# Kernel optimization log

Measured on AMD Instinct MI355X. Metric: run time of the kernel, lower is better.

The kernel has to match this reference:

```python
import jax, jax.numpy as jnp
import numpy as np

N = 262144          # total atoms
B = 2048            # graphs (batch.max()+1)
HID = 256           # hidden
CND = 128           # cond_proj_dim
K = 16              # n_clusters
PH = 8              # pool_heads
DH = HID // PH      # head_dim


def setup_inputs() -> dict:
    key = jax.random.key(0)
    ks = jax.random.split(key, 20)
    s = 0.02
    inp = {
        "h_atom": jax.random.normal(ks[0], (N, HID), jnp.float32),
        "c_atom": jax.random.normal(ks[1], (N, CND), jnp.float32),
        "batch": jnp.sort(jax.random.randint(ks[2], (N,), 0, B)).astype(jnp.int64),
        # gate: Linear(HID+CND, HID) -> GELU -> Linear(HID, 1) -> Sigmoid
        "W1": jax.random.normal(ks[3], (HID + CND, HID), jnp.float32) * s,
        "b1": jnp.zeros((HID,), jnp.float32),
        "W2": jax.random.normal(ks[4], (HID, 1), jnp.float32) * s,
        "b2": jnp.zeros((1,), jnp.float32),
        # assign: Linear(HID, HID) -> GELU -> Linear(HID, K)
        "A1": jax.random.normal(ks[5], (HID, HID), jnp.float32) * s,
        "ab1": jnp.zeros((HID,), jnp.float32),
        "A2": jax.random.normal(ks[6], (HID, K), jnp.float32) * s,
        "ab2": jnp.zeros((K,), jnp.float32),
        # cluster_proj: Linear(HID, HID)
        "Wc": jax.random.normal(ks[7], (HID, HID), jnp.float32) * s,
        "bc": jnp.zeros((HID,), jnp.float32),
        # readout
        "q": jax.random.normal(ks[8], (PH, DH), jnp.float32),   # readout_q param
        "Wk": jax.random.normal(ks[9], (HID, HID), jnp.float32) * s,
        "Wv": jax.random.normal(ks[10], (HID, HID), jnp.float32) * s,
        # LayerNorm
        "gamma": jnp.ones((HID,), jnp.float32),
        "beta": jnp.zeros((HID,), jnp.float32),
    }
    return inp


def reference(h_atom, c_atom, batch, W1, b1, W2, b2, A1, ab1, A2, ab2,
              Wc, bc, q, Wk, Wv, gamma, beta):
    gelu = lambda x: jax.nn.gelu(x, approximate=False)  # torch default GELU (erf)
    # Stage 1: condition-aware gating
    g = gelu(jnp.concatenate([h_atom, c_atom], axis=-1) @ W1 + b1)
    alpha = jax.nn.sigmoid(g @ W2 + b2)                 # [N, 1]
    h_gated = alpha * h_atom                            # [N, HID]
    # Stage 2: soft cluster assignment
    S = jax.nn.softmax(gelu(h_gated @ A1 + ab1) @ A2 + ab2, axis=-1)  # [N, K]
    # Ragged per-graph segment matmul: cluster[b,k,:] = sum_{n in graph b} S[n,k] * h_gated[n,:]
    cluster = jnp.stack(
        [jax.ops.segment_sum(h_gated * S[:, k:k + 1], batch, num_segments=B)
         for k in range(K)], axis=1)                    # [B, K, HID]
    cluster = cluster @ Wc + bc                         # cluster_proj
    # Stage 3: multi-head attention readout over K clusters
    Kp = (cluster @ Wk).reshape(B, K, PH, DH)
    Vp = (cluster @ Wv).reshape(B, K, PH, DH)
    scale = DH ** -0.5
    logits = jnp.einsum('pd,bkpd->bpk', q, Kp) * scale  # [B, PH, K]
    w = jax.nn.softmax(logits, axis=-1)                 # dropout p=0 -> identity
    out = jnp.einsum('bpk,bkpd->bpd', w, Vp).reshape(B, HID)
    # LayerNorm (eps = 1e-5, torch default)
    mu = out.mean(axis=-1, keepdims=True)
    var = ((out - mu) ** 2).mean(axis=-1, keepdims=True)
    return (out - mu) * jax.lax.rsqrt(var + 1e-5) * gamma + beta
```

## Files before the change

### kernel.cpp

```cpp
#include <hip/hip_runtime.h>
#include <hip/hip_bf16.h>
#include <math.h>

#define NATOMS 262144
#define BGRAPH 2048

typedef __bf16 bf16_t;
typedef __bf16 bf16x8 __attribute__((ext_vector_type(8)));
typedef __bf16 bf16x4 __attribute__((ext_vector_type(4)));
typedef float f32x4 __attribute__((ext_vector_type(4)));

__device__ __forceinline__ float bf2f(bf16_t x){ return (float)x; }
__device__ __forceinline__ float gelu_f(float x){ return 0.5f*x*(1.0f+erff(x*0.70710678118654752f)); }

__global__ void bounds_kernel(const int* __restrict__ batch,
                              const unsigned* __restrict__ gamma,
                              int* __restrict__ starts, int* __restrict__ flags) {
    if (blockIdx.x == 0 && threadIdx.x == 0)
        flags[0] = (gamma[0] == 0x3F803F80u) ? 1 : 0;
    int b = blockIdx.x * 256 + threadIdx.x;
    if (b > BGRAPH) return;
    int is64 = (batch[NATOMS - 1] == 0) ? 1 : 0;
    int lo = 0, hi = NATOMS;
    while (lo < hi) {
        int mid = (lo + hi) >> 1;
        int v = is64 ? batch[2 * mid] : batch[mid];
        if (v < b) lo = mid + 1; else hi = mid;
    }
    starts[b] = lo;
}

__global__ void params_kernel(const void* b1, const void* W2, const void* ab1,
                              const void* bc, const void* q, const void* gamma,
                              const void* beta, const void* ab2, const void* b2,
                              float* __restrict__ P, const int* __restrict__ flags) {
    int t = threadIdx.x;
    int bf = flags[0];
#define CV(p,i) (bf ? bf2f(((const bf16_t*)(p))[i]) : ((const float*)(p))[i])
    P[t]        = CV(b1, t);
    P[256 + t]  = CV(W2, t);
    P[512 + t]  = CV(ab1, t);
    P[768 + t]  = CV(bc, t);
    P[1024 + t] = CV(q, t);
    P[1280 + t] = CV(gamma, t);
    P[1536 + t] = CV(beta, t);
    if (t < 16) P[1792 + t] = CV(ab2, t);
    if (t == 16) P[1808] = CV(b2, 0);
#undef CV
}

__global__ void chunk_transpose(const void* __restrict__ src, bf16_t* __restrict__ dst,
                                int Kd, int Nn, const int* __restrict__ flags) {
    int i = blockIdx.x * 256 + threadIdx.x;
    if (i >= Kd * Nn) return;
    int k = i / Nn, n = i - k * Nn;
    bf16_t v = flags[0] ? ((const bf16_t*)src)[i] : (bf16_t)(((const float*)src)[i]);
    dst[((size_t)(k >> 5) * Nn + n) * 32 + (k & 31)] = v;
}

__global__ void a2_transpose(const void* __restrict__ src, bf16_t* __restrict__ dst,
                             const int* __restrict__ flags) {
    int i = blockIdx.x * 256 + threadIdx.x;
    if (i >= 256 * 16) return;
    int k = i >> 4, n = i & 15;
    bf16_t v = flags[0] ? ((const bf16_t*)src)[i] : (bf16_t)(((const float*)src)[i]);
    dst[n * 256 + k] = v;
}

__global__ __launch_bounds__(256, 2) void atom_kernel(
    const void* __restrict__ h, const void* __restrict__ cnd,
    const bf16_t* __restrict__ W1c, const bf16_t* __restrict__ A1c,
    const bf16_t* __restrict__ A2t, const float* __restrict__ P,
    const int* __restrict__ flags,
    bf16_t* __restrict__ hg_out, float* __restrict__ S_out)
{
    __shared__ bf16_t ldsX[64 * 392];
    __shared__ bf16_t ldsW[256 * 40];
    __shared__ float  ldsV[256];
    __shared__ float  ldsB1[256];
    __shared__ float  ldsAB1[256];
    __shared__ float  ldsAlpha[64];

    const int tid  = threadIdx.x;
    const int wave = tid >> 6;
    const int lane = tid & 63;
    const int quad = lane >> 4;
    const int l15  = lane & 15;
    const int a0   = blockIdx.x * 64;
    const int dbf  = flags[0];

    ldsV[tid]   = P[256 + tid];
    ldsB1[tid]  = P[tid];
    ldsAB1[tid] = P[512 + tid];
    if (tid < 64) ldsAlpha[tid] = 0.f;
    const float b2v = P[1808];

    if (dbf) {
        const uint4* hs = (const uint4*)((const bf16_t*)h + (size_t)a0 * 256);
        for (int i = 0; i < 8; ++i) {
            int lin = i * 256 + tid; int row = lin >> 5; int off = lin & 31;
            *(uint4*)(&ldsX[row * 392 + off * 8]) = hs[row * 32 + off];
        }
        const uint4* cs = (const uint4*)((const bf16_t*)cnd + (size_t)a0 * 128);
        for (int i = 0; i < 4; ++i) {
            int lin = i * 256 + tid; int row = lin >> 4; int off = lin & 15;
            *(uint4*)(&ldsX[row * 392 + 256 + off * 8]) = cs[row * 16 + off];
        }
    } else {
        const float4* hs = (const float4*)((const float*)h + (size_t)a0 * 256);
        for (int i = 0; i < 16; ++i) {
            int lin = i * 256 + tid; int row = lin >> 6; int off = lin & 63;
            float4 v = hs[row * 64 + off];
            bf16x4 w = { (bf16_t)v.x, (bf16_t)v.y, (bf16_t)v.z, (bf16_t)v.w };
            *(bf16x4*)(&ldsX[row * 392 + off * 4]) = w;
        }
        const float4* cs = (const float4*)((const float*)cnd + (size_t)a0 * 128);
        for (int i = 0; i < 8; ++i) {
            int lin = i * 256 + tid; int row = lin >> 5; int off = lin & 31;
            float4 v = cs[row * 32 + off];
            bf16x4 w = { (bf16_t)v.x, (bf16_t)v.y, (bf16_t)v.z, (bf16_t)v.w };
            *(bf16x4*)(&ldsX[row * 392 + 256 + off * 4]) = w;
        }
    }
    __syncthreads();

    f32x4 acc[4][4];
    for (int a = 0; a < 4; ++a) for (int b = 0; b < 4; ++b) acc[a][b] = (f32x4){0.f,0.f,0.f,0.f};

    for (int ks = 0; ks < 12; ++ks) {
        const uint4* src = (const uint4*)(W1c + (size_t)ks * 8192);
        for (int i = 0; i < 4; ++i) {
            int lin = i * 256 + tid; int n = lin >> 2, p = lin & 3;
            *(uint4*)(&ldsW[n * 40 + p * 8]) = src[n * 4 + p];
        }
        __syncthreads();
        bf16x8 af[4], bv[4];
        int kb = ks * 32 + quad * 8;
        for (int mt = 0; mt < 4; ++mt) af[mt] = *(const bf16x8*)(&ldsX[(mt * 16 + l15) * 392 + kb]);
        for (int j = 0; j < 4; ++j)   bv[j]  = *(const bf16x8*)(&ldsW[(wave * 64 + j * 16 + l15) * 40 + quad * 8]);
        for (int mt = 0; mt < 4; ++mt)
            for (int j = 0; j < 4; ++j)
                acc[mt][j] = __builtin_amdgcn_mfma_f32_16x16x32_bf16(af[mt], bv[j], acc[mt][j], 0, 0, 0);
        __syncthreads();
    }

    for (int mt = 0; mt < 4; ++mt) {
        float p[4] = {0.f, 0.f, 0.f, 0.f};
        for (int j = 0; j < 4; ++j) {
            int col = wave * 64 + j * 16 + l15;
            float w = ldsV[col];
            float bb = ldsB1[col];
            for (int r = 0; r < 4; ++r) {
                float g = gelu_f(acc[mt][j][r] + bb);
                p[r] += g * w;
            }
        }
        for (int off = 1; off < 16; off <<= 1)
            for (int r = 0; r < 4; ++r) p[r] += __shfl_xor(p[r], off, 64);
        if (l15 == 0)
            for (int r = 0; r < 4; ++r)
                atomicAdd(&ldsAlpha[mt * 16 + quad * 4 + r], p[r]);
    }
    __syncthreads();

    {
        int r = tid >> 2, p4 = tid & 3;
        float al = 1.f / (1.f + expf(-(ldsAlpha[r] + b2v)));
        bf16_t* xrow = &ldsX[r * 392 + p4 * 64];
        bf16_t* grow = hg_out + (size_t)(a0 + r) * 256 + p4 * 64;
        for (int i = 0; i < 8; ++i) {
            bf16x8 v = *(bf16x8*)(xrow + i * 8);
            for (int e = 0; e < 8; ++e) v[e] = (bf16_t)(bf2f(v[e]) * al);
            *(bf16x8*)(xrow + i * 8) = v;
            *(bf16x8*)(grow + i * 8) = v;
        }
    }
    __syncthreads();

    for (int a = 0; a < 4; ++a) for (int b = 0; b < 4; ++b) acc[a][b] = (f32x4){0.f,0.f,0.f,0.f};
    for (int ks = 0; ks < 8; ++ks) {
        const uint4* src = (const uint4*)(A1c + (size_t)ks * 8192);
        for (int i = 0; i < 4; ++i) {
            int lin = i * 256 + tid; int n = lin >> 2, p = lin & 3;
            *(uint4*)(&ldsW[n * 40 + p * 8]) = src[n * 4 + p];
        }
        __syncthreads();
        bf16x8 af[4], bv[4];
        int kb = ks * 32 + quad * 8;
        for (int mt = 0; mt < 4; ++mt) af[mt] = *(const bf16x8*)(&ldsX[(mt * 16 + l15) * 392 + kb]);
        for (int j = 0; j < 4; ++j)   bv[j]  = *(const bf16x8*)(&ldsW[(wave * 64 + j * 16 + l15) * 40 + quad * 8]);
        for (int mt = 0; mt < 4; ++mt)
            for (int j = 0; j < 4; ++j)
                acc[mt][j] = __builtin_amdgcn_mfma_f32_16x16x32_bf16(af[mt], bv[j], acc[mt][j], 0, 0, 0);
        __syncthreads();
    }

    for (int mt = 0; mt < 4; ++mt)
        for (int j = 0; j < 4; ++j) {
            int col = wave * 64 + j * 16 + l15;
            float bb = ldsAB1[col];
            for (int r = 0; r < 4; ++r) {
                int row = mt * 16 + quad * 4 + r;
                ldsX[row * 392 + col] = (bf16_t)gelu_f(acc[mt][j][r] + bb);
            }
        }
    if (tid < 128) {
        int n = tid >> 3, k0 = (tid & 7) * 32;
        for (int p = 0; p < 4; ++p)
            *(uint4*)(&ldsW[n * 264 + k0 + p * 8]) = *(const uint4*)(A2t + n * 256 + k0 + p * 8);
    }
    __syncthreads();

    f32x4 acc3 = (f32x4){0.f,0.f,0.f,0.f};
    for (int ks = 0; ks < 8; ++ks) {
        int kb = ks * 32 + quad * 8;
        bf16x8 a = *(const bf16x8*)(&ldsX[(wave * 16 + l15) * 392 + kb]);
        bf16x8 b = *(const bf16x8*)(&ldsW[l15 * 264 + kb]);
        acc3 = __builtin_amdgcn_mfma_f32_16x16x32_bf16(a, b, acc3, 0, 0, 0);
    }
    float ab2v = P[1792 + l15];
    float lv[4], mx[4], ex[4], sm[4];
    for (int r = 0; r < 4; ++r) { lv[r] = acc3[r] + ab2v; mx[r] = lv[r]; }
    for (int off = 1; off < 16; off <<= 1)
        for (int r = 0; r < 4; ++r) { float o = __shfl_xor(mx[r], off, 64); mx[r] = fmaxf(mx[r], o); }
    for (int r = 0; r < 4; ++r) { ex[r] = expf(lv[r] - mx[r]); sm[r] = ex[r]; }
    for (int off = 1; off < 16; off <<= 1)
        for (int r = 0; r < 4; ++r) sm[r] += __shfl_xor(sm[r], off, 64);
    for (int r = 0; r < 4; ++r) {
        int row = wave * 16 + quad * 4 + r;
        S_out[(size_t)(a0 + row) * 16 + l15] = ex[r] / sm[r];
    }
}

__global__ __launch_bounds__(256) void segment_kernel(
    const bf16_t* __restrict__ hg, const float* __restrict__ S,
    const int* __restrict__ starts, bf16_t* __restrict__ craw)
{
    __shared__ float ldsS[16 * 16];
    int b = blockIdx.x, tid = threadIdx.x;
    int s = starts[b], e = starts[b + 1];
    float acc[16];
#pragma unroll
    for (int k = 0; k < 16; ++k) acc[k] = 0.f;
    for (int n0 = s; n0 < e; n0 += 16) {
        int cnt = min(16, e - n0);
        if (tid < cnt * 16) ldsS[tid] = S[(size_t)(n0 + (tid >> 4)) * 16 + (tid & 15)];
        __syncthreads();
        for (int a = 0; a < cnt; ++a) {
            float v = bf2f(hg[(size_t)(n0 + a) * 256 + tid]);
            const f32x4* sr = (const f32x4*)(&ldsS[a * 16]);
            f32x4 s0 = sr[0], s1 = sr[1], s2 = sr[2], s3 = sr[3];
            acc[0]  += s0[0] * v; acc[1]  += s0[1] * v; acc[2]  += s0[2] * v; acc[3]  += s0[3] * v;
            acc[4]  += s1[0] * v; acc[5]  += s1[1] * v; acc[6]  += s1[2] * v; acc[7]  += s1[3] * v;
            acc[8]  += s2[0] * v; acc[9]  += s2[1] * v; acc[10] += s2[2] * v; acc[11] += s2[3] * v;
            acc[12] += s3[0] * v; acc[13] += s3[1] * v; acc[14] += s3[2] * v; acc[15] += s3[3] * v;
        }
        __syncthreads();
    }
#pragma unroll
    for (int k = 0; k < 16; ++k)
        craw[((size_t)b * 16 + k) * 256 + tid] = (bf16_t)acc[k];
}

__global__ __launch_bounds__(256, 2) void gemm_kernel(
    const bf16_t* __restrict__ A, const bf16_t* __restrict__ Wck,
    const float* __restrict__ bias, bf16_t* __restrict__ C)
{
    __shared__ bf16_t ldsA[64 * 264];
    __shared__ bf16_t ldsW[256 * 40];
    const int tid = threadIdx.x;
    const int wave = tid >> 6, lane = tid & 63, quad = lane >> 4, l15 = lane & 15;
    const size_t r0 = (size_t)blockIdx.x * 64;

    const uint4* as = (const uint4*)(A + r0 * 256);
    for (int i = 0; i < 8; ++i) {
        int lin = i * 256 + tid; int row = lin >> 5; int off = lin & 31;
        *(uint4*)(&ldsA[row * 264 + off * 8]) = as[row * 32 + off];
    }
    f32x4 acc[4][4];
    for (int a = 0; a < 4; ++a) for (int b = 0; b < 4; ++b) acc[a][b] = (f32x4){0.f,0.f,0.f,0.f};

    for (int ks = 0; ks < 8; ++ks) {
        const uint4* src = (const uint4*)(Wck + (size_t)ks * 8192);
        for (int i = 0; i < 4; ++i) {
            int lin = i * 256 + tid; int n = lin >> 2, p = lin & 3;
            *(uint4*)(&ldsW[n * 40 + p * 8]) = src[n * 4 + p];
        }
        __syncthreads();
        bf16x8 af[4], bv[4];
        int kb = ks * 32 + quad * 8;
        for (int mt = 0; mt < 4; ++mt) af[mt] = *(const bf16x8*)(&ldsA[(mt * 16 + l15) * 264 + kb]);
        for (int j = 0; j < 4; ++j)   bv[j]  = *(const bf16x8*)(&ldsW[(wave * 64 + j * 16 + l15) * 40 + quad * 8]);
        for (int mt = 0; mt < 4; ++mt)
            for (int j = 0; j < 4; ++j)
                acc[mt][j] = __builtin_amdgcn_mfma_f32_16x16x32_bf16(af[mt], bv[j], acc[mt][j], 0, 0, 0);
        __syncthreads();
    }
    for (int mt = 0; mt < 4; ++mt)
        for (int j = 0; j < 4; ++j) {
            int col = wave * 64 + j * 16 + l15;
            float bvl = bias ? bias[col] : 0.f;
            for (int r = 0; r < 4; ++r)
                C[(r0 + mt * 16 + quad * 4 + r) * 256 + col] = (bf16_t)(acc[mt][j][r] + bvl);
        }
}

__global__ __launch_bounds__(256) void attn_ln_kernel(
    const bf16_t* __restrict__ Kp, const bf16_t* __restrict__ Vp,
    const float* __restrict__ P, const int* __restrict__ flags,
    void* __restrict__ out)
{
    __shared__ float lw[8][16];
    __shared__ float w1s[4], w2s[4];
    int b = blockIdx.x, tid = threadIdx.x;
    const int dbf = flags[0];
    const float* q     = P + 1024;
    const float* gamma = P + 1280;
    const float* beta  = P + 1536;
    if (tid < 128) {
        int p = tid >> 4, k = tid & 15;
        const bf16_t* kr = Kp + ((size_t)b * 16 + k) * 256 + p * 32;
        const float* qr = q + p * 32;
        float dot = 0.f;
        for (int d = 0; d < 32; ++d) dot += qr[d] * bf2f(kr[d]);
        lw[p][k] = dot * 0.17677669529663687f;
    }
    __syncthreads();
    if (tid < 8) {
        float m = -1e30f;
        for (int k = 0; k < 16; ++k) m = fmaxf(m, lw[tid][k]);
        float s = 0.f;
        for (int k = 0; k < 16; ++k) { float ev = expf(lw[tid][k] - m); lw[tid][k] = ev; s += ev; }
        float inv = 1.f / s;
        for (int k = 0; k < 16; ++k) lw[tid][k] *= inv;
    }
    __syncthreads();
    int p = tid >> 5, d = tid & 31;
    float o = 0.f;
    for (int k = 0; k < 16; ++k)
        o += lw[p][k] * bf2f(Vp[((size_t)b * 16 + k) * 256 + p * 32 + d]);
    float s1 = o, s2 = o * o;
    for (int off = 1; off < 64; off <<= 1) { s1 += __shfl_xor(s1, off, 64); s2 += __shfl_xor(s2, off, 64); }
    int wv = tid >> 6;
    if ((tid & 63) == 0) { w1s[wv] = s1; w2s[wv] = s2; }
    __syncthreads();
    float ts1 = w1s[0] + w1s[1] + w1s[2] + w1s[3];
    float ts2 = w2s[0] + w2s[1] + w2s[2] + w2s[3];
    float mu = ts1 * (1.f / 256.f);
    float var = ts2 * (1.f / 256.f) - mu * mu;
    float y = (o - mu) * rsqrtf(var + 1e-5f) * gamma[tid] + beta[tid];
    if (dbf) ((bf16_t*)out)[(size_t)b * 256 + tid] = (bf16_t)y;
    else     ((float*)out)[(size_t)b * 256 + tid]  = y;
}

extern "C" void kernel_launch(void* const* d_in, const int* in_sizes, int n_in,
                              void* d_out, int out_size, void* d_ws, size_t ws_size,
                              hipStream_t stream) {
    const void* h     = d_in[0];
    const void* cnd   = d_in[1];
    const int*  batch = (const int*)d_in[2];
    const void* W1    = d_in[3];
    const void* b1    = d_in[4];
    const void* W2    = d_in[5];
    const void* b2    = d_in[6];
    const void* A1    = d_in[7];
    const void* ab1   = d_in[8];
    const void* A2    = d_in[9];
    const void* ab2   = d_in[10];
    const void* Wc    = d_in[11];
    const void* bc    = d_in[12];
    const void* q     = d_in[13];
    const void* Wk    = d_in[14];
    const void* Wv    = d_in[15];
    const void* gamma = d_in[16];
    const void* beta  = d_in[17];

    char* ws = (char*)d_ws;
    size_t off = 0;
    bf16_t* W1c  = (bf16_t*)(ws + off); off += 196608;
    bf16_t* A1c  = (bf16_t*)(ws + off); off += 131072;
    bf16_t* Wcc  = (bf16_t*)(ws + off); off += 131072;
    bf16_t* Wkc  = (bf16_t*)(ws + off); off += 131072;
    bf16_t* Wvc  = (bf16_t*)(ws + off); off += 131072;
    bf16_t* A2t  = (bf16_t*)(ws + off); off += 8192;
    float*  P    = (float*)(ws + off);  off += 8192;
    int*    flags = (int*)(ws + off);   off += 256;
    int*    starts = (int*)(ws + off);  off += 8448;
    float*  S    = (float*)(ws + off);  off += (size_t)NATOMS * 16 * 4;
    bf16_t* hg   = (bf16_t*)(ws + off); off += (size_t)NATOMS * 256 * 2;
    bf16_t* craw = (bf16_t*)(ws + off); off += (size_t)BGRAPH * 16 * 256 * 2;
    bf16_t* cP   = (bf16_t*)(ws + off); off += (size_t)BGRAPH * 16 * 256 * 2;
    bf16_t* KpB  = (bf16_t*)(ws + off); off += (size_t)BGRAPH * 16 * 256 * 2;
    bf16_t* VpB  = (bf16_t*)(ws + off); off += (size_t)BGRAPH * 16 * 256 * 2;
    (void)ws_size; (void)n_in; (void)in_sizes; (void)out_size;

    bounds_kernel<<<9, 256, 0, stream>>>(batch, (const unsigned*)gamma, starts, flags);
    params_kernel<<<1, 256, 0, stream>>>(b1, W2, ab1, bc, q, gamma, beta, ab2, b2, P, flags);
    chunk_transpose<<<(384 * 256 + 255) / 256, 256, 0, stream>>>(W1, W1c, 384, 256, flags);
    chunk_transpose<<<(256 * 256 + 255) / 256, 256, 0, stream>>>(A1, A1c, 256, 256, flags);
    chunk_transpose<<<(256 * 256 + 255) / 256, 256, 0, stream>>>(Wc, Wcc, 256, 256, flags);
    chunk_transpose<<<(256 * 256 + 255) / 256, 256, 0, stream>>>(Wk, Wkc, 256, 256, flags);
    chunk_transpose<<<(256 * 256 + 255) / 256, 256, 0, stream>>>(Wv, Wvc, 256, 256, flags);
    a2_transpose<<<16, 256, 0, stream>>>(A2, A2t, flags);

    atom_kernel<<<NATOMS / 64, 256, 0, stream>>>(h, cnd, W1c, A1c, A2t, P, flags, hg, S);
    segment_kernel<<<BGRAPH, 256, 0, stream>>>(hg, S, starts, craw);
    gemm_kernel<<<BGRAPH * 16 / 64, 256, 0, stream>>>(craw, Wcc, P + 768, cP);
    gemm_kernel<<<BGRAPH * 16 / 64, 256, 0, stream>>>(cP, Wkc, nullptr, KpB);
    gemm_kernel<<<BGRAPH * 16 / 64, 256, 0, stream>>>(cP, Wvc, nullptr, VpB);
    attn_ln_kernel<<<BGRAPH, 256, 0, stream>>>(KpB, VpB, P, flags, d_out);
}
```

Before: 839.3 us.

## Double-buffer weight tiles via direct global-to-LDS loads, fuse K/V GEMMs

Weight chunks are pre-padded to a 40-element stride so they can be copied straight into LDS with global_load_lds, double-buffered so the next chunk loads while MFMAs run on the current one. The conditioning input is converted to bf16 in a separate pre-pass and held in registers, which shrinks the atom tile's LDS footprint. The Wk and Wv projections are merged into one kernel that reuses the staged activation tile, and MFMA sections are wrapped in setprio. The changes add a c_convert pass over c_atom, raise register pressure from the cached fragments, and reuse the craw buffer as scratch for the converted input.

```diff
diff --git a/kernel.cpp b/kernel.cpp
--- a/kernel.cpp
+++ b/kernel.cpp
@@ -1,9 +1,11 @@
 #include <hip/hip_runtime.h>
 #include <hip/hip_bf16.h>
 #include <math.h>
+#include <stdint.h>
 
 #define NATOMS 262144
 #define BGRAPH 2048
+#define CHUNK 10240
 
 typedef __bf16 bf16_t;
 typedef __bf16 bf16x8 __attribute__((ext_vector_type(8)));
@@ -12,6 +14,13 @@
 
 __device__ __forceinline__ float bf2f(bf16_t x){ return (float)x; }
 __device__ __forceinline__ float gelu_f(float x){ return 0.5f*x*(1.0f+erff(x*0.70710678118654752f)); }
+
+__device__ __forceinline__ void gl_lds16(const void* g, void* l){
+    __attribute__((address_space(3))) uint32_t* lp =
+        reinterpret_cast<__attribute__((address_space(3))) uint32_t*>(
+            reinterpret_cast<uintptr_t>(l));
+    __builtin_amdgcn_global_load_lds(static_cast<const uint32_t*>(g), lp, 16, 0, 0);
+}
 
 __global__ void bounds_kernel(const int* __restrict__ batch,
                               const unsigned* __restrict__ gamma,
@@ -55,7 +64,7 @@
     if (i >= Kd * Nn) return;
     int k = i / Nn, n = i - k * Nn;
     bf16_t v = flags[0] ? ((const bf16_t*)src)[i] : (bf16_t)(((const float*)src)[i]);
-    dst[((size_t)(k >> 5) * Nn + n) * 32 + (k & 31)] = v;
+    dst[((size_t)(k >> 5) * Nn + n) * 40 + (k & 31)] = v;
 }
 
 __global__ void a2_transpose(const void* __restrict__ src, bf16_t* __restrict__ dst,
@@ -67,15 +76,28 @@
     dst[n * 256 + k] = v;
 }
 
+__global__ void c_convert(const float* __restrict__ c, bf16_t* __restrict__ cb,
+                          const int* __restrict__ flags) {
+    if (flags[0]) return;
+    const size_t total = (size_t)NATOMS * 128 / 8;
+    for (size_t i = (size_t)blockIdx.x * 256 + threadIdx.x; i < total; i += (size_t)2048 * 256) {
+        const float4* s = (const float4*)c + i * 2;
+        float4 a = s[0], b = s[1];
+        bf16x8 v = { (bf16_t)a.x,(bf16_t)a.y,(bf16_t)a.z,(bf16_t)a.w,
+                     (bf16_t)b.x,(bf16_t)b.y,(bf16_t)b.z,(bf16_t)b.w };
+        *(bf16x8*)(cb + i * 8) = v;
+    }
+}
+
 __global__ __launch_bounds__(256, 2) void atom_kernel(
-    const void* __restrict__ h, const void* __restrict__ cnd,
+    const void* __restrict__ h, const void* __restrict__ cnd, const bf16_t* __restrict__ cb,
     const bf16_t* __restrict__ W1c, const bf16_t* __restrict__ A1c,
     const bf16_t* __restrict__ A2t, const float* __restrict__ P,
     const int* __restrict__ flags,
     bf16_t* __restrict__ hg_out, float* __restrict__ S_out)
 {
-    __shared__ bf16_t ldsX[64 * 392];
-    __shared__ bf16_t ldsW[256 * 40];
+    __shared__ bf16_t ldsX[64 * 264];
+    __shared__ bf16_t ldsW[2][CHUNK];
     __shared__ float  ldsV[256];
     __shared__ float  ldsB1[256];
     __shared__ float  ldsAB1[256];
@@ -89,6 +111,15 @@
     const int a0   = blockIdx.x * 64;
     const int dbf  = flags[0];
 
+    const bf16_t* cbp = dbf ? (const bf16_t*)cnd : cb;
+
+    bf16x8 cf[4][4];
+#pragma unroll
+    for (int kc = 0; kc < 4; ++kc)
+#pragma unroll
+        for (int mt = 0; mt < 4; ++mt)
+            cf[kc][mt] = *(const bf16x8*)(cbp + (size_t)(a0 + mt * 16 + l15) * 128 + kc * 32 + quad * 8);
+
     ldsV[tid]   = P[256 + tid];
     ldsB1[tid]  = P[tid];
     ldsAB1[tid] = P[512 + tid];
@@ -97,50 +128,63 @@
 
     if (dbf) {
         const uint4* hs = (const uint4*)((const bf16_t*)h + (size_t)a0 * 256);
+#pragma unroll
         for (int i = 0; i < 8; ++i) {
             int lin = i * 256 + tid; int row = lin >> 5; int off = lin & 31;
-            *(uint4*)(&ldsX[row * 392 + off * 8]) = hs[row * 32 + off];
-        }
-        const uint4* cs = (const uint4*)((const bf16_t*)cnd + (size_t)a0 * 128);
-        for (int i = 0; i < 4; ++i) {
-            int lin = i * 256 + tid; int row = lin >> 4; int off = lin & 15;
-            *(uint4*)(&ldsX[row * 392 + 256 + off * 8]) = cs[row * 16 + off];
+            *(uint4*)(&ldsX[row * 264 + off * 8]) = hs[row * 32 + off];
         }
     } else {
         const float4* hs = (const float4*)((const float*)h + (size_t)a0 * 256);
+#pragma unroll
         for (int i = 0; i < 16; ++i) {
             int lin = i * 256 + tid; int row = lin >> 6; int off = lin & 63;
             float4 v = hs[row * 64 + off];
             bf16x4 w = { (bf16_t)v.x, (bf16_t)v.y, (bf16_t)v.z, (bf16_t)v.w };
-            *(bf16x4*)(&ldsX[row * 392 + off * 4]) = w;
-        }
-        const float4* cs = (const float4*)((const float*)cnd + (size_t)a0 * 128);
-        for (int i = 0; i < 8; ++i) {
-            int lin = i * 256 + tid; int row = lin >> 5; int off = lin & 31;
-            float4 v = cs[row * 32 + off];
-            bf16x4 w = { (bf16_t)v.x, (bf16_t)v.y, (bf16_t)v.z, (bf16_t)v.w };
-            *(bf16x4*)(&ldsX[row * 392 + 256 + off * 4]) = w;
-        }
-    }
+            *(bf16x4*)(&ldsX[row * 264 + off * 4]) = w;
+        }
+    }
+
+    auto stage = [&](int bsel, const bf16_t* src){
+#pragma unroll
+        for (int i = 0; i < 5; ++i) {
+            int u = i * 256 + wave * 64;
+            gl_lds16(src + (size_t)(u + lane) * 8, &ldsW[bsel][u * 8]);
+        }
+    };
+
+    stage(0, W1c);
     __syncthreads();
 
     f32x4 acc[4][4];
-    for (int a = 0; a < 4; ++a) for (int b = 0; b < 4; ++b) acc[a][b] = (f32x4){0.f,0.f,0.f,0.f};
-
+#pragma unroll
+    for (int a = 0; a < 4; ++a)
+#pragma unroll
+        for (int b = 0; b < 4; ++b) acc[a][b] = (f32x4){0.f,0.f,0.f,0.f};
+
+#pragma unroll
     for (int ks = 0; ks < 12; ++ks) {
-        const uint4* src = (const uint4*)(W1c + (size_t)ks * 8192);
-        for (int i = 0; i < 4; ++i) {
-            int lin = i * 256 + tid; int n = lin >> 2, p = lin & 3;
-            *(uint4*)(&ldsW[n * 40 + p * 8]) = src[n * 4 + p];
-        }
-        __syncthreads();
+        const int cur = ks & 1;
+        const bf16_t* nxt = (ks < 11) ? (W1c + (size_t)(ks + 1) * CHUNK) : A1c;
+        stage(cur ^ 1, nxt);
         bf16x8 af[4], bv[4];
-        int kb = ks * 32 + quad * 8;
-        for (int mt = 0; mt < 4; ++mt) af[mt] = *(const bf16x8*)(&ldsX[(mt * 16 + l15) * 392 + kb]);
-        for (int j = 0; j < 4; ++j)   bv[j]  = *(const bf16x8*)(&ldsW[(wave * 64 + j * 16 + l15) * 40 + quad * 8]);
+#pragma unroll
+        for (int j = 0; j < 4; ++j)
+            bv[j] = *(const bf16x8*)(&ldsW[cur][(wave * 64 + j * 16 + l15) * 40 + quad * 8]);
+        if (ks < 8) {
+            int kb = ks * 32 + quad * 8;
+#pragma unroll
+            for (int mt = 0; mt < 4; ++mt) af[mt] = *(const bf16x8*)(&ldsX[(mt * 16 + l15) * 264 + kb]);
+        } else {
+#pragma unroll
+            for (int mt = 0; mt < 4; ++mt) af[mt] = cf[ks - 8][mt];
+        }
+        __builtin_amdgcn_s_setprio(1);
+#pragma unroll
         for (int mt = 0; mt < 4; ++mt)
+#pragma unroll
             for (int j = 0; j < 4; ++j)
                 acc[mt][j] = __builtin_amdgcn_mfma_f32_16x16x32_bf16(af[mt], bv[j], acc[mt][j], 0, 0, 0);
+        __builtin_amdgcn_s_setprio(0);
         __syncthreads();
     }
 
@@ -166,7 +210,7 @@
     {
         int r = tid >> 2, p4 = tid & 3;
         float al = 1.f / (1.f + expf(-(ldsAlpha[r] + b2v)));
-        bf16_t* xrow = &ldsX[r * 392 + p4 * 64];
+        bf16_t* xrow = &ldsX[r * 264 + p4 * 64];
         bf16_t* grow = hg_out + (size_t)(a0 + r) * 256 + p4 * 64;
         for (int i = 0; i < 8; ++i) {
             bf16x8 v = *(bf16x8*)(xrow + i * 8);
@@ -177,21 +221,28 @@
     }
     __syncthreads();
 
-    for (int a = 0; a < 4; ++a) for (int b = 0; b < 4; ++b) acc[a][b] = (f32x4){0.f,0.f,0.f,0.f};
+#pragma unroll
+    for (int a = 0; a < 4; ++a)
+#pragma unroll
+        for (int b = 0; b < 4; ++b) acc[a][b] = (f32x4){0.f,0.f,0.f,0.f};
+#pragma unroll
     for (int ks = 0; ks < 8; ++ks) {
-        const uint4* src = (const uint4*)(A1c + (size_t)ks * 8192);
-        for (int i = 0; i < 4; ++i) {
-            int lin = i * 256 + tid; int n = lin >> 2, p = lin & 3;
-            *(uint4*)(&ldsW[n * 40 + p * 8]) = src[n * 4 + p];
-        }
-        __syncthreads();
+        const int cur = ks & 1;
+        if (ks < 7) stage(cur ^ 1, A1c + (size_t)(ks + 1) * CHUNK);
         bf16x8 af[4], bv[4];
         int kb = ks * 32 + quad * 8;
-        for (int mt = 0; mt < 4; ++mt) af[mt] = *(const bf16x8*)(&ldsX[(mt * 16 + l15) * 392 + kb]);
-        for (int j = 0; j < 4; ++j)   bv[j]  = *(const bf16x8*)(&ldsW[(wave * 64 + j * 16 + l15) * 40 + quad * 8]);
+#pragma unroll
+        for (int j = 0; j < 4; ++j)
+            bv[j] = *(const bf16x8*)(&ldsW[cur][(wave * 64 + j * 16 + l15) * 40 + quad * 8]);
+#pragma unroll
+        for (int mt = 0; mt < 4; ++mt) af[mt] = *(const bf16x8*)(&ldsX[(mt * 16 + l15) * 264 + kb]);
+        __builtin_amdgcn_s_setprio(1);
+#pragma unroll
         for (int mt = 0; mt < 4; ++mt)
+#pragma unroll
             for (int j = 0; j < 4; ++j)
                 acc[mt][j] = __builtin_amdgcn_mfma_f32_16x16x32_bf16(af[mt], bv[j], acc[mt][j], 0, 0, 0);
+        __builtin_amdgcn_s_setprio(0);
         __syncthreads();
     }
 
@@ -201,21 +252,23 @@
             float bb = ldsAB1[col];
             for (int r = 0; r < 4; ++r) {
                 int row = mt * 16 + quad * 4 + r;
-                ldsX[row * 392 + col] = (bf16_t)gelu_f(acc[mt][j][r] + bb);
+                ldsX[row * 264 + col] = (bf16_t)gelu_f(acc[mt][j][r] + bb);
             }
         }
     if (tid < 128) {
         int n = tid >> 3, k0 = (tid & 7) * 32;
+#pragma unroll
         for (int p = 0; p < 4; ++p)
-            *(uint4*)(&ldsW[n * 264 + k0 + p * 8]) = *(const uint4*)(A2t + n * 256 + k0 + p * 8);
+            *(uint4*)(&ldsW[0][n * 264 + k0 + p * 8]) = *(const uint4*)(A2t + n * 256 + k0 + p * 8);
     }
     __syncthreads();
 
     f32x4 acc3 = (f32x4){0.f,0.f,0.f,0.f};
+#pragma unroll
     for (int ks = 0; ks < 8; ++ks) {
         int kb = ks * 32 + quad * 8;
-        bf16x8 a = *(const bf16x8*)(&ldsX[(wave * 16 + l15) * 392 + kb]);
-        bf16x8 b = *(const bf16x8*)(&ldsW[l15 * 264 + kb]);
+        bf16x8 a = *(const bf16x8*)(&ldsX[(wave * 16 + l15) * 264 + kb]);
+        bf16x8 b = *(const bf16x8*)(&ldsW[0][l15 * 264 + kb]);
         acc3 = __builtin_amdgcn_mfma_f32_16x16x32_bf16(a, b, acc3, 0, 0, 0);
     }
     float ab2v = P[1792 + l15];
@@ -267,33 +320,52 @@
     const float* __restrict__ bias, bf16_t* __restrict__ C)
 {
     __shared__ bf16_t ldsA[64 * 264];
-    __shared__ bf16_t ldsW[256 * 40];
+    __shared__ bf16_t ldsW[2][CHUNK];
     const int tid = threadIdx.x;
     const int wave = tid >> 6, lane = tid & 63, quad = lane >> 4, l15 = lane & 15;
     const size_t r0 = (size_t)blockIdx.x * 64;
 
+    auto stage = [&](int bsel, const bf16_t* src){
+#pragma unroll
+        for (int i = 0; i < 5; ++i) {
+            int u = i * 256 + wave * 64;
+            gl_lds16(src + (size_t)(u + lane) * 8, &ldsW[bsel][u * 8]);
+        }
+    };
+
     const uint4* as = (const uint4*)(A + r0 * 256);
+#pragma unroll
     for (int i = 0; i < 8; ++i) {
         int lin = i * 256 + tid; int row = lin >> 5; int off = lin & 31;
         *(uint4*)(&ldsA[row * 264 + off * 8]) = as[row * 32 + off];
     }
+    stage(0, Wck);
+    __syncthreads();
+
     f32x4 acc[4][4];
-    for (int a = 0; a < 4; ++a) for (int b = 0; b < 4; ++b) acc[a][b] = (f32x4){0.f,0.f,0.f,0.f};
-
+#pragma unroll
+    for (int a = 0; a < 4; ++a)
+#pragma unroll
+        for (int b = 0; b < 4; ++b) acc[a][b] = (f32x4){0.f,0.f,0.f,0.f};
+
+#pragma unroll
     for (int ks = 0; ks < 8; ++ks) {
-        const uint4* src = (const uint4*)(Wck + (size_t)ks * 8192);
-        for (int i = 0; i < 4; ++i) {
-            int lin = i * 256 + tid; int n = lin >> 2, p = lin & 3;
-            *(uint4*)(&ldsW[n * 40 + p * 8]) = src[n * 4 + p];
-        }
-        __syncthreads();
+        const int cur = ks & 1;
+        if (ks < 7) stage(cur ^ 1, Wck + (size_t)(ks + 1) * CHUNK);
         bf16x8 af[4], bv[4];
         int kb = ks * 32 + quad * 8;
+#pragma unroll
+        for (int j = 0; j < 4; ++j)
+            bv[j] = *(const bf16x8*)(&ldsW[cur][(wave * 64 + j * 16 + l15) * 40 + quad * 8]);
+#pragma unroll
         for (int mt = 0; mt < 4; ++mt) af[mt] = *(const bf16x8*)(&ldsA[(mt * 16 + l15) * 264 + kb]);
-        for (int j = 0; j < 4; ++j)   bv[j]  = *(const bf16x8*)(&ldsW[(wave * 64 + j * 16 + l15) * 40 + quad * 8]);
+        __builtin_amdgcn_s_setprio(1);
+#pragma unroll
         for (int mt = 0; mt < 4; ++mt)
+#pragma unroll
             for (int j = 0; j < 4; ++j)
                 acc[mt][j] = __builtin_amdgcn_mfma_f32_16x16x32_bf16(af[mt], bv[j], acc[mt][j], 0, 0, 0);
+        __builtin_amdgcn_s_setprio(0);
         __syncthreads();
     }
     for (int mt = 0; mt < 4; ++mt)
@@ -302,6 +374,99 @@
             float bvl = bias ? bias[col] : 0.f;
             for (int r = 0; r < 4; ++r)
                 C[(r0 + mt * 16 + quad * 4 + r) * 256 + col] = (bf16_t)(acc[mt][j][r] + bvl);
+        }
+}
+
+__global__ __launch_bounds__(256, 2) void gemm2x_kernel(
+    const bf16_t* __restrict__ A, const bf16_t* __restrict__ Wkc, const bf16_t* __restrict__ Wvc,
+    bf16_t* __restrict__ CK, bf16_t* __restrict__ CV)
+{
+    __shared__ bf16_t ldsA[64 * 264];
+    __shared__ bf16_t ldsW[2][CHUNK];
+    const int tid = threadIdx.x;
+    const int wave = tid >> 6, lane = tid & 63, quad = lane >> 4, l15 = lane & 15;
+    const size_t r0 = (size_t)blockIdx.x * 64;
+
+    auto stage = [&](int bsel, const bf16_t* src){
+#pragma unroll
+        for (int i = 0; i < 5; ++i) {
+            int u = i * 256 + wave * 64;
+            gl_lds16(src + (size_t)(u + lane) * 8, &ldsW[bsel][u * 8]);
+        }
+    };
+
+    const uint4* as = (const uint4*)(A + r0 * 256);
+#pragma unroll
+    for (int i = 0; i < 8; ++i) {
+        int lin = i * 256 + tid; int row = lin >> 5; int off = lin & 31;
+        *(uint4*)(&ldsA[row * 264 + off * 8]) = as[row * 32 + off];
+    }
+    stage(0, Wkc);
+    __syncthreads();
+
+    f32x4 acc[4][4];
+#pragma unroll
+    for (int a = 0; a < 4; ++a)
+#pragma unroll
+        for (int b = 0; b < 4; ++b) acc[a][b] = (f32x4){0.f,0.f,0.f,0.f};
+
+#pragma unroll
+    for (int ks = 0; ks < 8; ++ks) {
+        const int cur = ks & 1;
+        const bf16_t* nxt = (ks < 7) ? (Wkc + (size_t)(ks + 1) * CHUNK) : Wvc;
+        stage(cur ^ 1, nxt);
+        bf16x8 af[4], bv[4];
+        int kb = ks * 32 + quad * 8;
+#pragma unroll
+        for (int j = 0; j < 4; ++j)
+            bv[j] = *(const bf16x8*)(&ldsW[cur][(wave * 64 + j * 16 + l15) * 40 + quad * 8]);
+#pragma unroll
+        for (int mt = 0; mt < 4; ++mt) af[mt] = *(const bf16x8*)(&ldsA[(mt * 16 + l15) * 264 + kb]);
+        __builtin_amdgcn_s_setprio(1);
+#pragma unroll
+        for (int mt = 0; mt < 4; ++mt)
+#pragma unroll
+            for (int j = 0; j < 4; ++j)
+                acc[mt][j] = __builtin_amdgcn_mfma_f32_16x16x32_bf16(af[mt], bv[j], acc[mt][j], 0, 0, 0);
+        __builtin_amdgcn_s_setprio(0);
+        __syncthreads();
+    }
+    for (int mt = 0; mt < 4; ++mt)
+        for (int j = 0; j < 4; ++j) {
+            int col = wave * 64 + j * 16 + l15;
+            for (int r = 0; r < 4; ++r)
+                CK[(r0 + mt * 16 + quad * 4 + r) * 256 + col] = (bf16_t)acc[mt][j][r];
+        }
+
+#pragma unroll
+    for (int a = 0; a < 4; ++a)
+#pragma unroll
+        for (int b = 0; b < 4; ++b) acc[a][b] = (f32x4){0.f,0.f,0.f,0.f};
+#pragma unroll
+    for (int ks = 0; ks < 8; ++ks) {
+        const int cur = ks & 1;
+        if (ks < 7) stage(cur ^ 1, Wvc + (size_t)(ks + 1) * CHUNK);
+        bf16x8 af[4], bv[4];
+        int kb = ks * 32 + quad * 8;
+#pragma unroll
+        for (int j = 0; j < 4; ++j)
+            bv[j] = *(const bf16x8*)(&ldsW[cur][(wave * 64 + j * 16 + l15) * 40 + quad * 8]);
+#pragma unroll
+        for (int mt = 0; mt < 4; ++mt) af[mt] = *(const bf16x8*)(&ldsA[(mt * 16 + l15) * 264 + kb]);
+        __builtin_amdgcn_s_setprio(1);
+#pragma unroll
+        for (int mt = 0; mt < 4; ++mt)
+#pragma unroll
+            for (int j = 0; j < 4; ++j)
+                acc[mt][j] = __builtin_amdgcn_mfma_f32_16x16x32_bf16(af[mt], bv[j], acc[mt][j], 0, 0, 0);
+        __builtin_amdgcn_s_setprio(0);
+        __syncthreads();
+    }
+    for (int mt = 0; mt < 4; ++mt)
+        for (int j = 0; j < 4; ++j) {
+            int col = wave * 64 + j * 16 + l15;
+            for (int r = 0; r < 4; ++r)
+                CV[(r0 + mt * 16 + quad * 4 + r) * 256 + col] = (bf16_t)acc[mt][j][r];
         }
 }
 
@@ -319,10 +484,15 @@
     const float* beta  = P + 1536;
     if (tid < 128) {
         int p = tid >> 4, k = tid & 15;
-        const bf16_t* kr = Kp + ((size_t)b * 16 + k) * 256 + p * 32;
+        const bf16x8* kr = (const bf16x8*)(Kp + ((size_t)b * 16 + k) * 256 + p * 32);
         const float* qr = q + p * 32;
         float dot = 0.f;
-        for (int d = 0; d < 32; ++d) dot += qr[d] * bf2f(kr[d]);
+#pragma unroll
+        for (int i = 0; i < 4; ++i) {
+            bf16x8 v = kr[i];
+#pragma unroll
+            for (int e = 0; e < 8; ++e) dot += qr[i * 8 + e] * bf2f(v[e]);
+        }
         lw[p][k] = dot * 0.17677669529663687f;
     }
     __syncthreads();
@@ -377,11 +547,11 @@
 
     char* ws = (char*)d_ws;
     size_t off = 0;
-    bf16_t* W1c  = (bf16_t*)(ws + off); off += 196608;
-    bf16_t* A1c  = (bf16_t*)(ws + off); off += 131072;
-    bf16_t* Wcc  = (bf16_t*)(ws + off); off += 131072;
-    bf16_t* Wkc  = (bf16_t*)(ws + off); off += 131072;
-    bf16_t* Wvc  = (bf16_t*)(ws + off); off += 131072;
+    bf16_t* W1c  = (bf16_t*)(ws + off); off += 12 * CHUNK * 2;
+    bf16_t* A1c  = (bf16_t*)(ws + off); off += 8 * CHUNK * 2;
+    bf16_t* Wcc  = (bf16_t*)(ws + off); off += 8 * CHUNK * 2;
+    bf16_t* Wkc  = (bf16_t*)(ws + off); off += 8 * CHUNK * 2;
+    bf16_t* Wvc  = (bf16_t*)(ws + off); off += 8 * CHUNK * 2;
     bf16_t* A2t  = (bf16_t*)(ws + off); off += 8192;
     float*  P    = (float*)(ws + off);  off += 8192;
     int*    flags = (int*)(ws + off);   off += 256;
@@ -392,6 +562,7 @@
     bf16_t* cP   = (bf16_t*)(ws + off); off += (size_t)BGRAPH * 16 * 256 * 2;
     bf16_t* KpB  = (bf16_t*)(ws + off); off += (size_t)BGRAPH * 16 * 256 * 2;
     bf16_t* VpB  = (bf16_t*)(ws + off); off += (size_t)BGRAPH * 16 * 256 * 2;
+    bf16_t* cb   = craw;
     (void)ws_size; (void)n_in; (void)in_sizes; (void)out_size;
 
     bounds_kernel<<<9, 256, 0, stream>>>(batch, (const unsigned*)gamma, starts, flags);
@@ -402,11 +573,11 @@
     chunk_transpose<<<(256 * 256 + 255) / 256, 256, 0, stream>>>(Wk, Wkc, 256, 256, flags);
     chunk_transpose<<<(256 * 256 + 255) / 256, 256, 0, stream>>>(Wv, Wvc, 256, 256, flags);
     a2_transpose<<<16, 256, 0, stream>>>(A2, A2t, flags);
-
-    atom_kernel<<<NATOMS / 64, 256, 0, stream>>>(h, cnd, W1c, A1c, A2t, P, flags, hg, S);
+    c_convert<<<2048, 256, 0, stream>>>((const float*)cnd, cb, flags);
+
+    atom_kernel<<<NATOMS / 64, 256, 0, stream>>>(h, cnd, cb, W1c, A1c, A2t, P, flags, hg, S);
     segment_kernel<<<BGRAPH, 256, 0, stream>>>(hg, S, starts, craw);
     gemm_kernel<<<BGRAPH * 16 / 64, 256, 0, stream>>>(craw, Wcc, P + 768, cP);
-    gemm_kernel<<<BGRAPH * 16 / 64, 256, 0, stream>>>(cP, Wkc, nullptr, KpB);
-    gemm_kernel<<<BGRAPH * 16 / 64, 256, 0, stream>>>(cP, Wvc, nullptr, VpB);
+    gemm2x_kernel<<<BGRAPH * 16 / 64, 256, 0, stream>>>(cP, Wkc, Wvc, KpB, VpB);
     attn_ln_kernel<<<BGRAPH, 256, 0, stream>>>(KpB, VpB, P, flags, d_out);
 }
```

Measured after the change: 835.9 us. Within noise of the previous version (-0.4%).
